# Performance work log

Hardware: AMD Instinct MI355X
Metric: run time of the kernel (lower is better)

The kernel has to match this reference:

```python
import jax, jax.numpy as jnp
import numpy as np
from jax.scipy.special import logsumexp

DEN_SCALE = 1.0  # den_scale from LFMMILoss.__init__


def _log_marginal(em, seqlens, logA, log_start, log_final):
    """Forward (alpha) recursion of a WFSA in log space.
    em: [B,T,S] per-state emission log-likelihoods; logA: [S,S] or [B,S,S].
    Returns per-sequence log-marginal [B].
    """
    B, T, S = em.shape
    alpha0 = log_start + em[:, 0]  # [B,S]

    def step(alpha, xs):
        em_t, t = xs
        # [B,S,1] + [.,S,S] -> logsumexp over source state
        new = logsumexp(alpha[:, :, None] + logA, axis=1) + em_t
        alpha = jnp.where((t < seqlens)[:, None], new, alpha)
        return alpha, None

    em_t_first = jnp.swapaxes(em, 0, 1)  # [T,B,S]
    alpha, _ = jax.lax.scan(step, alpha0, (em_t_first[1:], jnp.arange(1, T)))
    return logsumexp(alpha + log_final, axis=1)  # [B]


def _fsm_logprob(x, seqlens, logA, log_start, log_final, pdf_ids):
    B, T, _ = x.shape
    if pdf_ids.ndim == 1:  # shared graph (denominator)
        em = x[:, :, pdf_ids]  # [B,T,S]
    else:  # per-utterance graphs (numerators), pdf_ids: [B,S]
        S = pdf_ids.shape[-1]
        idx = jnp.broadcast_to(pdf_ids[:, None, :], (B, T, S))
        em = jnp.take_along_axis(x, idx, axis=2)
    return _log_marginal(em, seqlens, logA, log_start, log_final)


def setup_inputs() -> dict:
    key = jax.random.key(0)
    ks = jax.random.split(key, 10)
    B, T, C = 16, 500, 2048
    S_num, S_den = 64, 512
    inp = jax.random.normal(ks[0], (B, T, C), jnp.float32)
    seqlengths = jax.random.randint(ks[1], (B,), T // 2, T + 1, jnp.int32)
    num_logA = jax.nn.log_softmax(jax.random.normal(ks[2], (B, S_num, S_num), jnp.float32), axis=-1)
    num_log_start = jax.nn.log_softmax(jax.random.normal(ks[3], (B, S_num), jnp.float32), axis=-1)
    num_log_final = jax.nn.log_softmax(jax.random.normal(ks[4], (B, S_num), jnp.float32), axis=-1)
    num_pdf_ids = jax.random.randint(ks[5], (B, S_num), 0, C, jnp.int32)
    den_logA = jax.nn.log_softmax(jax.random.normal(ks[6], (S_den, S_den), jnp.float32), axis=-1)
    den_log_start = jax.nn.log_softmax(jax.random.normal(ks[7], (S_den,), jnp.float32), axis=-1)
    den_log_final = jax.nn.log_softmax(jax.random.normal(ks[8], (S_den,), jnp.float32), axis=-1)
    den_pdf_ids = jax.random.randint(ks[9], (S_den,), 0, C, jnp.int32)
    return {
        "input": inp, "seqlengths": seqlengths,
        "num_logA": num_logA, "num_log_start": num_log_start,
        "num_log_final": num_log_final, "num_pdf_ids": num_pdf_ids,
        "den_logA": den_logA, "den_log_start": den_log_start,
        "den_log_final": den_log_final, "den_pdf_ids": den_pdf_ids,
    }


def reference(input, seqlengths, num_logA, num_log_start, num_log_final,
              num_pdf_ids, den_logA, den_log_start, den_log_final, den_pdf_ids):
    x = jnp.clip(input, -30.0, 30.0)
    num_llh = _fsm_logprob(x, seqlengths, num_logA, num_log_start, num_log_final, num_pdf_ids).sum()
    den_llh = _fsm_logprob(x, seqlengths, den_logA, den_log_start, den_log_final, den_pdf_ids).sum()
    return -(num_llh - DEN_SCALE * den_llh)
```

## Files before the change

### kernel.cpp

```cpp
#include <hip/hip_runtime.h>
#include <math.h>

#define BB 16
#define TT 500
#define CC 2048
#define SN 64
#define SD 512
#define NGRP 16
#define NCB 8
#define NDEN 128
#define NTHR 512
#define SHIFTC 30.0f

#define WSF_DACC   32768
#define WSF_DSCALE 32784
#define WSF_NACC   32800
#define WSF_NSCALE 32816

#define AL(p) __hip_atomic_load((p), __ATOMIC_RELAXED, __HIP_MEMORY_SCOPE_AGENT)
#define AS(p, v) __hip_atomic_store((p), (v), __ATOMIC_RELAXED, __HIP_MEMORY_SCOPE_AGENT)

__device__ __forceinline__ float wave_max(float v) {
  #pragma unroll
  for (int off = 32; off > 0; off >>= 1) v = fmaxf(v, __shfl_xor(v, off, 64));
  return v;
}
__device__ __forceinline__ float wave_sum(float v) {
  #pragma unroll
  for (int off = 32; off > 0; off >>= 1) v += __shfl_xor(v, off, 64);
  return v;
}
__device__ __forceinline__ unsigned long long pk(unsigned tag, float v) {
  return ((unsigned long long)tag << 32) | (unsigned long long)__float_as_uint(v);
}
__device__ __forceinline__ float clamp30(float v) {
  return fminf(fmaxf(v, -30.f), 30.f);
}

__global__ __launch_bounds__(NTHR, 1) void fsm_fwd(
    const float* __restrict__ x, const int* __restrict__ seqlens,
    const float* __restrict__ nA, const float* __restrict__ nls,
    const float* __restrict__ nlf, const int* __restrict__ npdf,
    const float* __restrict__ dA, const float* __restrict__ dls,
    const float* __restrict__ dlf, const int* __restrict__ dpdf,
    unsigned long long* __restrict__ p64, float* __restrict__ wsf)
{
  __shared__ float prt[2][8 * 64];
  __shared__ float pmx[2][8];
  const int tid = threadIdx.x;
  const int lane = tid & 63, wv = tid >> 6;

  if (blockIdx.x < NDEN) {
    const int g  = blockIdx.x & 15;
    const int cb = blockIdx.x >> 4;
    const int j0 = cb * 64;

    float Areg[64];
    {
      const float* Ap = dA + (wv * 64) * SD + j0 + lane;
      #pragma unroll
      for (int k = 0; k < 64; ++k)
        Areg[k] = __expf(Ap[k * SD]);
    }

    unsigned long long* gb0 = p64 + (size_t)g * SD;
    unsigned long long* gb1 = p64 + (size_t)(NGRP + g) * SD;

    int pdfj = 0, sl = 0; float lfj = 0.f, pcur = 0.f, scale = SHIFTC;
    if (wv == 0) {
      pdfj = dpdf[j0 + lane];
      lfj  = dlf[j0 + lane];
      sl   = seqlens[g];
      float xv = clamp30(x[g * (TT * CC) + pdfj]);
      pcur = __expf(dls[j0 + lane] + xv - SHIFTC);
      AS(gb0 + j0 + lane, pk(0u, pcur));
    }

    for (int t = 1; t < TT; ++t) {
      unsigned long long* gin  = (t & 1) ? gb0 : gb1;
      unsigned long long* gout = (t & 1) ? gb1 : gb0;
      float xv = 0.f;
      if (wv == 0)
        xv = clamp30(x[g * (TT * CC) + t * CC + pdfj]);

      const unsigned tg = (unsigned)(t - 1);
      unsigned long long* pa = gin + wv * 64 + lane;
      unsigned long long w;
      for (;;) {
        w = AL(pa);
        if ((unsigned)(w >> 32) == tg) break;
        __builtin_amdgcn_s_sleep(1);
      }
      float pv = __uint_as_float((unsigned)w);

      float cm = wave_max(pv);
      if (lane == 0) pmx[t & 1][wv] = cm;

      float q = 0.f;
      #pragma unroll
      for (int k = 0; k < 64; ++k) {
        float pk_ = __uint_as_float(__builtin_amdgcn_readlane(__float_as_uint(pv), k));
        q = fmaf(pk_, Areg[k], q);
      }
      prt[t & 1][wv * 64 + lane] = q;
      __syncthreads();

      if (wv == 0) {
        const float* pb = prt[t & 1];
        float qq = 0.f;
        #pragma unroll
        for (int w8 = 0; w8 < 8; ++w8) qq += pb[w8 * 64 + lane];
        float m = pmx[t & 1][0];
        #pragma unroll
        for (int w8 = 1; w8 < 8; ++w8) m = fmaxf(m, pmx[t & 1][w8]);
        float lm = __logf(m);
        if (t < sl) {
          pcur = qq * __expf(xv - SHIFTC - lm);
          scale += SHIFTC + lm;
        }
        AS(gout + j0 + lane, pk((unsigned)t, pcur));
      }
    }
    if (wv == 0) {
      float part = wave_sum(pcur * __expf(lfj));
      if (lane == 0) {
        atomicAdd(wsf + WSF_DACC + g, part);
        if (cb == 0) wsf[WSF_DSCALE + g] = scale;
      }
    }
  } else {
    const int b = blockIdx.x - NDEN;
    if (wv != 0) return;

    float Areg[64];
    {
      const float* Ap = nA + b * SN * SN + lane;
      #pragma unroll
      for (int i = 0; i < 64; ++i)
        Areg[i] = __expf(Ap[i * SN]);
    }
    const int   pdfj = npdf[b * SN + lane];
    const float lfj  = nlf[b * SN + lane];
    const int   sl   = seqlens[b];
    float xv = clamp30(x[b * (TT * CC) + pdfj]);
    float pcur = __expf(nls[b * SN + lane] + xv - SHIFTC);
    float scale = SHIFTC;

    for (int t = 1; t < TT; ++t) {
      xv = clamp30(x[b * (TT * CC) + t * CC + pdfj]);
      float pold = pcur;
      float q = 0.f;
      #pragma unroll
      for (int i = 0; i < 64; ++i) {
        float pi = __uint_as_float(__builtin_amdgcn_readlane(__float_as_uint(pold), i));
        q = fmaf(pi, Areg[i], q);
      }
      float lm = __logf(wave_max(pold));
      if (t < sl) {
        pcur = q * __expf(xv - SHIFTC - lm);
        scale += SHIFTC + lm;
      }
    }
    float part = wave_sum(pcur * __expf(lfj));
    if (lane == 0) {
      wsf[WSF_NACC + b]   = part;
      wsf[WSF_NSCALE + b] = scale;
    }
  }
}

__global__ void fsm_final(const float* __restrict__ wsf, float* __restrict__ out) {
  const int tid = threadIdx.x;
  float v = 0.f;
  if (tid < 16)
    v = -(wsf[WSF_NSCALE + tid] + __logf(wsf[WSF_NACC + tid]));
  else if (tid < 32)
    v = (wsf[WSF_DSCALE + tid - 16] + __logf(wsf[WSF_DACC + tid - 16]));
  v = wave_sum(v);
  if (tid == 0) out[0] = v;
}

extern "C" void kernel_launch(void* const* d_in, const int* in_sizes, int n_in,
                              void* d_out, int out_size, void* d_ws, size_t ws_size,
                              hipStream_t stream) {
  const float* x    = (const float*)d_in[0];
  const int*   sql  = (const int*)d_in[1];
  const float* nA   = (const float*)d_in[2];
  const float* nls  = (const float*)d_in[3];
  const float* nlf  = (const float*)d_in[4];
  const int*   npdf = (const int*)d_in[5];
  const float* dA   = (const float*)d_in[6];
  const float* dls  = (const float*)d_in[7];
  const float* dlf  = (const float*)d_in[8];
  const int*   dpdf = (const int*)d_in[9];
  float* out = (float*)d_out;
  unsigned long long* p64 = (unsigned long long*)d_ws;
  float* wsf = (float*)d_ws;
  (void)in_sizes; (void)n_in; (void)out_size; (void)ws_size;

  hipMemsetAsync((char*)d_ws + 131072, 0, 256, stream);
  fsm_fwd<<<NDEN + BB, NTHR, 0, stream>>>(x, sql, nA, nls, nlf, npdf,
                                          dA, dls, dlf, dpdf, p64, wsf);
  fsm_final<<<1, 64, 0, stream>>>(wsf, out);
}
```

Baseline: 873.5 us.

## Interleave four sequences per denominator workgroup with prefetched state polling

Denominator work now uses 32 workgroups, each handling four sequences round-robin instead of one sequence per workgroup. While one sequence waits on cross-workgroup state, the others make progress. Wave 0 takes a smaller slice of source states (22) because it also does the normalization and publish step; the other waves take 70 each. Next-step state words and emissions are prefetched, and the numerator path also prefetches the next emission. The aim is to hide global synchronization latency, at the cost of more serial work per workgroup, more register pressure, and a more complex polling protocol.

```diff
diff --git a/kernel.cpp b/kernel.cpp
--- a/kernel.cpp
+++ b/kernel.cpp
@@ -7,10 +7,13 @@
 #define SN 64
 #define SD 512
 #define NGRP 16
-#define NCB 8
-#define NDEN 128
+#define GPW 4
+#define NSETS 4
+#define NDENWG 32
 #define NTHR 512
 #define SHIFTC 30.0f
+#define K0 22
+#define KO 70
 
 #define WSF_DACC   32768
 #define WSF_DSCALE 32784
@@ -35,6 +38,16 @@
 }
 __device__ __forceinline__ float clamp30(float v) {
   return fminf(fmaxf(v, -30.f), 30.f);
+}
+__device__ __forceinline__ float lo32(unsigned long long w) {
+  return __uint_as_float((unsigned)w);
+}
+__device__ __forceinline__ float rlane(float v, int k) {
+  return __uint_as_float(__builtin_amdgcn_readlane(__float_as_uint(v), k));
+}
+__device__ __forceinline__ unsigned long long* recbase(
+    unsigned long long* p64, int g, int tag) {
+  return p64 + ((tag & 1) ? (size_t)(NGRP + g) : (size_t)g) * SD;
 }
 
 __global__ __launch_bounds__(NTHR, 1) void fsm_fwd(
@@ -45,91 +58,140 @@
     const float* __restrict__ dlf, const int* __restrict__ dpdf,
     unsigned long long* __restrict__ p64, float* __restrict__ wsf)
 {
-  __shared__ float prt[2][8 * 64];
+  __shared__ float prt[2][8][64];
   __shared__ float pmx[2][8];
   const int tid = threadIdx.x;
   const int lane = tid & 63, wv = tid >> 6;
 
-  if (blockIdx.x < NDEN) {
-    const int g  = blockIdx.x & 15;
-    const int cb = blockIdx.x >> 4;
+  if (blockIdx.x < NDENWG) {
+    const int gs = blockIdx.x >> 3;
+    const int cb = blockIdx.x & 7;
     const int j0 = cb * 64;
-
-    float Areg[64];
-    {
-      const float* Ap = dA + (wv * 64) * SD + j0 + lane;
-      #pragma unroll
-      for (int k = 0; k < 64; ++k)
-        Areg[k] = __expf(Ap[k * SD]);
-    }
-
-    unsigned long long* gb0 = p64 + (size_t)g * SD;
-    unsigned long long* gb1 = p64 + (size_t)(NGRP + g) * SD;
-
-    int pdfj = 0, sl = 0; float lfj = 0.f, pcur = 0.f, scale = SHIFTC;
+    const int gbase = gs * GPW;
+
     if (wv == 0) {
-      pdfj = dpdf[j0 + lane];
-      lfj  = dlf[j0 + lane];
-      sl   = seqlens[g];
-      float xv = clamp30(x[g * (TT * CC) + pdfj]);
-      pcur = __expf(dls[j0 + lane] + xv - SHIFTC);
-      AS(gb0 + j0 + lane, pk(0u, pcur));
-    }
-
-    for (int t = 1; t < TT; ++t) {
-      unsigned long long* gin  = (t & 1) ? gb0 : gb1;
-      unsigned long long* gout = (t & 1) ? gb1 : gb0;
-      float xv = 0.f;
-      if (wv == 0)
-        xv = clamp30(x[g * (TT * CC) + t * CC + pdfj]);
-
-      const unsigned tg = (unsigned)(t - 1);
-      unsigned long long* pa = gin + wv * 64 + lane;
-      unsigned long long w;
-      for (;;) {
-        w = AL(pa);
-        if ((unsigned)(w >> 32) == tg) break;
-        __builtin_amdgcn_s_sleep(1);
-      }
-      float pv = __uint_as_float((unsigned)w);
-
-      float cm = wave_max(pv);
-      if (lane == 0) pmx[t & 1][wv] = cm;
-
-      float q = 0.f;
-      #pragma unroll
-      for (int k = 0; k < 64; ++k) {
-        float pk_ = __uint_as_float(__builtin_amdgcn_readlane(__float_as_uint(pv), k));
-        q = fmaf(pk_, Areg[k], q);
-      }
-      prt[t & 1][wv * 64 + lane] = q;
-      __syncthreads();
-
-      if (wv == 0) {
-        const float* pb = prt[t & 1];
-        float qq = 0.f;
+      float Areg[K0];
+      #pragma unroll
+      for (int k = 0; k < K0; ++k)
+        Areg[k] = __expf(dA[k * SD + j0 + lane]);
+      const int   pdfj = dpdf[j0 + lane];
+      const float lfj  = dlf[j0 + lane];
+      int sl[GPW]; float pcur[GPW], scale[GPW];
+      #pragma unroll
+      for (int gk = 0; gk < GPW; ++gk) {
+        const int g = gbase + gk;
+        sl[gk] = seqlens[g];
+        float xv = clamp30(x[g * (TT * CC) + pdfj]);
+        pcur[gk]  = __expf(dls[j0 + lane] + xv - SHIFTC);
+        scale[gk] = SHIFTC;
+        AS(recbase(p64, g, 0) + j0 + lane, pk(0u, pcur[gk]));
+      }
+      unsigned long long st = AL(recbase(p64, gbase, 0) + lane);
+      float xnext = clamp30(x[gbase * (TT * CC) + CC + pdfj]);
+
+      for (int t = 1; t < TT; ++t) {
         #pragma unroll
-        for (int w8 = 0; w8 < 8; ++w8) qq += pb[w8 * 64 + lane];
-        float m = pmx[t & 1][0];
-        #pragma unroll
-        for (int w8 = 1; w8 < 8; ++w8) m = fmaxf(m, pmx[t & 1][w8]);
-        float lm = __logf(m);
-        if (t < sl) {
-          pcur = qq * __expf(xv - SHIFTC - lm);
-          scale += SHIFTC + lm;
+        for (int gk = 0; gk < GPW; ++gk) {
+          const int g  = gbase + gk;
+          const int tn = (gk == GPW - 1) ? t + 1 : t;
+          const int gn = gbase + ((gk + 1) & (GPW - 1));
+          unsigned long long w0 = st;
+          float xv = xnext;
+          if (tn < TT) {
+            st    = AL(recbase(p64, gn, tn - 1) + lane);
+            xnext = clamp30(x[gn * (TT * CC) + tn * CC + pdfj]);
+          }
+          const unsigned tg = (unsigned)(t - 1);
+          unsigned long long* pa = recbase(p64, g, t - 1) + lane;
+          bool ok = (lane >= K0) || ((unsigned)(w0 >> 32) == tg);
+          while (!__all(ok)) {
+            __builtin_amdgcn_s_sleep(1);
+            w0 = AL(pa);
+            ok = (lane >= K0) || ((unsigned)(w0 >> 32) == tg);
+          }
+          float pv = lo32(w0);
+          float cm = wave_max((lane < K0) ? pv : 0.f);
+          if (lane == 0) pmx[gk & 1][0] = cm;
+          float q = 0.f;
+          #pragma unroll
+          for (int k = 0; k < K0; ++k)
+            q = fmaf(rlane(pv, k), Areg[k], q);
+          prt[gk & 1][0][lane] = q;
+          __syncthreads();
+          float qq = 0.f;
+          #pragma unroll
+          for (int w8 = 0; w8 < 8; ++w8) qq += prt[gk & 1][w8][lane];
+          float m = pmx[gk & 1][0];
+          #pragma unroll
+          for (int w8 = 1; w8 < 8; ++w8) m = fmaxf(m, pmx[gk & 1][w8]);
+          float lm = __logf(m);
+          if (t < sl[gk]) {
+            pcur[gk] = qq * __expf(xv - SHIFTC - lm);
+            scale[gk] += SHIFTC + lm;
+          }
+          AS(recbase(p64, g, t) + j0 + lane, pk((unsigned)t, pcur[gk]));
         }
-        AS(gout + j0 + lane, pk((unsigned)t, pcur));
-      }
-    }
-    if (wv == 0) {
-      float part = wave_sum(pcur * __expf(lfj));
-      if (lane == 0) {
-        atomicAdd(wsf + WSF_DACC + g, part);
-        if (cb == 0) wsf[WSF_DSCALE + g] = scale;
+      }
+      #pragma unroll
+      for (int gk = 0; gk < GPW; ++gk) {
+        const int g = gbase + gk;
+        float part = wave_sum(pcur[gk] * __expf(lfj));
+        if (lane == 0) {
+          atomicAdd(wsf + WSF_DACC + g, part);
+          if (cb == 0) wsf[WSF_DSCALE + g] = scale[gk];
+        }
+      }
+    } else {
+      const int kb = K0 + (wv - 1) * KO;
+      float Areg[KO];
+      #pragma unroll
+      for (int k = 0; k < KO; ++k)
+        Areg[k] = __expf(dA[(kb + k) * SD + j0 + lane]);
+      const int i0 = kb + lane;
+      int i1 = kb + 64 + lane; if (i1 > SD - 1) i1 = SD - 1;
+      unsigned long long s0 = AL(recbase(p64, gbase, 0) + i0);
+      unsigned long long s1 = AL(recbase(p64, gbase, 0) + i1);
+
+      for (int t = 1; t < TT; ++t) {
+        #pragma unroll 1
+        for (int gk = 0; gk < GPW; ++gk) {
+          const int g  = gbase + gk;
+          const int tn = (gk == GPW - 1) ? t + 1 : t;
+          const int gn = gbase + ((gk + 1) & (GPW - 1));
+          unsigned long long w0 = s0, w1 = s1;
+          if (tn < TT) {
+            unsigned long long* nb = recbase(p64, gn, tn - 1);
+            s0 = AL(nb + i0);
+            s1 = AL(nb + i1);
+          }
+          const unsigned tg = (unsigned)(t - 1);
+          unsigned long long* cbse = recbase(p64, g, t - 1);
+          bool ok = ((unsigned)(w0 >> 32) == tg) &&
+                    (lane >= (KO - 64) || (unsigned)(w1 >> 32) == tg);
+          while (!__all(ok)) {
+            __builtin_amdgcn_s_sleep(1);
+            w0 = AL(cbse + i0);
+            w1 = AL(cbse + i1);
+            ok = ((unsigned)(w0 >> 32) == tg) &&
+                 (lane >= (KO - 64) || (unsigned)(w1 >> 32) == tg);
+          }
+          float pv0 = lo32(w0), pv1 = lo32(w1);
+          float cm = wave_max(fmaxf(pv0, (lane < (KO - 64)) ? pv1 : 0.f));
+          if (lane == 0) pmx[gk & 1][wv] = cm;
+          float q = 0.f;
+          #pragma unroll
+          for (int k = 0; k < 64; ++k)
+            q = fmaf(rlane(pv0, k), Areg[k], q);
+          #pragma unroll
+          for (int k = 64; k < KO; ++k)
+            q = fmaf(rlane(pv1, k - 64), Areg[k], q);
+          prt[gk & 1][wv][lane] = q;
+          __syncthreads();
+        }
       }
     }
   } else {
-    const int b = blockIdx.x - NDEN;
+    const int b = blockIdx.x - NDENWG;
     if (wv != 0) return;
 
     float Areg[64];
@@ -142,17 +204,20 @@
     const int   pdfj = npdf[b * SN + lane];
     const float lfj  = nlf[b * SN + lane];
     const int   sl   = seqlens[b];
-    float xv = clamp30(x[b * (TT * CC) + pdfj]);
-    float pcur = __expf(nls[b * SN + lane] + xv - SHIFTC);
+    float xv0 = clamp30(x[b * (TT * CC) + pdfj]);
+    float pcur = __expf(nls[b * SN + lane] + xv0 - SHIFTC);
     float scale = SHIFTC;
+    float xn = clamp30(x[b * (TT * CC) + CC + pdfj]);
 
     for (int t = 1; t < TT; ++t) {
-      xv = clamp30(x[b * (TT * CC) + t * CC + pdfj]);
+      float xv = xn;
+      if (t + 1 < TT)
+        xn = clamp30(x[b * (TT * CC) + (t + 1) * CC + pdfj]);
       float pold = pcur;
       float q = 0.f;
       #pragma unroll
       for (int i = 0; i < 64; ++i) {
-        float pi = __uint_as_float(__builtin_amdgcn_readlane(__float_as_uint(pold), i));
+        float pi = rlane(pold, i);
         q = fmaf(pi, Areg[i], q);
       }
       float lm = __logf(wave_max(pold));
@@ -199,7 +264,7 @@
   (void)in_sizes; (void)n_in; (void)out_size; (void)ws_size;
 
   hipMemsetAsync((char*)d_ws + 131072, 0, 256, stream);
-  fsm_fwd<<<NDEN + BB, NTHR, 0, stream>>>(x, sql, nA, nls, nlf, npdf,
-                                          dA, dls, dlf, dpdf, p64, wsf);
+  fsm_fwd<<<NDENWG + BB, NTHR, 0, stream>>>(x, sql, nA, nls, nlf, npdf,
+                                            dA, dls, dlf, dpdf, p64, wsf);
   fsm_final<<<1, 64, 0, stream>>>(wsf, out);
 }
```

New measurement: 2.116 ms. 2.42x slower.
